# Kernel optimization log

Hardware: AMD Instinct MI355X
Metric: run time of the kernel (lower is better)

## Reference

```python
import jax, jax.numpy as jnp
import numpy as np

B, D, L, K = 8, 256, 2048, 24
R = L // 2 + 1  # rfft bins
H = 2 * D      # mlp hidden
EPS = 1e-5


def setup_inputs() -> dict:
    key = jax.random.key(0)
    ks = jax.random.split(key, 10)
    s_theta = 1.0 / np.sqrt(D)   # ~kaiming_uniform scale
    s_w1 = 1.0 / np.sqrt(D)
    s_w2 = 1.0 / np.sqrt(H)
    return {
        "x": jax.random.normal(ks[0], (B, D, L), dtype=jnp.float32),
        "Phi_f_re": jax.random.normal(ks[1], (K, R), dtype=jnp.float32),
        "Phi_f_im": jax.random.normal(ks[2], (K, R), dtype=jnp.float32),
        "Theta": jax.random.uniform(ks[3], (K, D, D), jnp.float32, -s_theta, s_theta),
        "gamma": jnp.ones((D,), jnp.float32),
        "beta": jnp.zeros((D,), jnp.float32),
        "W1": jax.random.uniform(ks[4], (H, D), jnp.float32, -s_w1, s_w1),
        "b1": jax.random.uniform(ks[5], (H,), jnp.float32, -s_w1, s_w1),
        "W2": jax.random.uniform(ks[6], (D, H), jnp.float32, -s_w2, s_w2),
        "b2": jax.random.uniform(ks[7], (D,), jnp.float32, -s_w2, s_w2),
    }


def reference(x, Phi_f_re, Phi_f_im, Theta, gamma, beta, W1, b1, W2, b2):
    # x: [B, D, L]. LayerNorm over channel dim D (torch norms last dim of x.transpose(1,2)).
    mu = jnp.mean(x, axis=1, keepdims=True)
    var = jnp.var(x, axis=1, keepdims=True)
    z = (x - mu) * jax.lax.rsqrt(var + EPS) * gamma[None, :, None] + beta[None, :, None]

    Xf = jnp.fft.rfft(z, axis=-1)                       # [B, D, R] complex
    Phi_c = Phi_f_re - 1j * Phi_f_im                    # conj(Phi_f), [K, R]
    # Sf[b,h,r] = sum_{d,k} Xf[b,d,r] * conj(Phi)[k,r] * Theta[k,h,d]
    # (identical to the torch real/imag split since Theta is real)
    Sf = jnp.einsum('bdr,kr,khd->bhr', Xf, Phi_c, Theta)
    S = jnp.fft.irfft(Sf, n=L, axis=-1)                 # [B, D, L]

    # 1x1 Conv1d MLP with exact GELU
    h = jax.nn.gelu(jnp.einsum('hd,bdl->bhl', W1, S) + b1[None, :, None], approximate=False)
    out = jnp.einsum('dh,bhl->bdl', W2, h) + b2[None, :, None]
    return x + out
```

## Files before the change

### kernel.cpp

```cpp
#include <hip/hip_runtime.h>
#include <hip/hip_bf16.h>
#include <hip/hip_fp16.h>
#include <math.h>

#define BB 8
#define DD 256
#define LL 2048
#define KK 24
#define RR 1025
#define HH 512

typedef __attribute__((ext_vector_type(8))) _Float16 f16x8;
typedef __attribute__((ext_vector_type(4))) float f32x4;

__device__ __forceinline__ unsigned short f2h(float f) {
  return __builtin_bit_cast(unsigned short, __float2half_rn(f));
}

__global__ void ln_kernel(const float* __restrict__ x, const float* __restrict__ gamma,
                          const float* __restrict__ beta, float* __restrict__ z) {
  __shared__ float red[2][4][64];
  __shared__ float mu_s[64], rs_s[64];
  int blk = blockIdx.x;
  int b = blk >> 5;
  int l0 = (blk & 31) << 6;
  int t = threadIdx.x;
  int ll = t & 63;
  int part = t >> 6;
  int l = l0 + ll;
  const float* xb = x + ((size_t)b * DD) * LL + l;
  float xv[64];
  float s = 0.f, ss = 0.f;
  #pragma unroll
  for (int i = 0; i < 64; ++i) {
    float v = xb[(size_t)(part * 64 + i) * LL];
    xv[i] = v; s += v; ss += v * v;
  }
  red[0][part][ll] = s; red[1][part][ll] = ss;
  __syncthreads();
  if (part == 0) {
    float S = red[0][0][ll] + red[0][1][ll] + red[0][2][ll] + red[0][3][ll];
    float Q = red[1][0][ll] + red[1][1][ll] + red[1][2][ll] + red[1][3][ll];
    float mu = S * (1.f / 256.f);
    float var = Q * (1.f / 256.f) - mu * mu;
    mu_s[ll] = mu; rs_s[ll] = rsqrtf(var + 1e-5f);
  }
  __syncthreads();
  float mu = mu_s[ll], rs = rs_s[ll];
  float* zb = z + ((size_t)b * DD) * LL + l;
  #pragma unroll
  for (int i = 0; i < 64; ++i) {
    int d = part * 64 + i;
    zb[(size_t)d * LL] = (xv[i] - mu) * rs * gamma[d] + beta[d];
  }
}

__global__ void theta_prep(const float* __restrict__ Theta, unsigned* __restrict__ A2u) {
  int bi = blockIdx.x;
  int k = bi >> 8, h = bi & 255;
  int t = threadIdx.x;
  float2 v = *reinterpret_cast<const float2*>(Theta + (size_t)k * 65536 + h * 256 + 2 * t);
  A2u[(size_t)h * 3072 + k * 128 + t] =
      __builtin_bit_cast(unsigned, __floats2half2_rn(v.x, v.y));
}

__global__ void w_prep(const float* __restrict__ W1, const float* __restrict__ W2,
                       unsigned* __restrict__ W1h, unsigned* __restrict__ W2h) {
  int i = blockIdx.x * 256 + threadIdx.x;
  float2 a = reinterpret_cast<const float2*>(W1)[i];
  W1h[i] = __builtin_bit_cast(unsigned, __floats2half2_rn(a.x, a.y));
  float2 b = reinterpret_cast<const float2*>(W2)[i];
  W2h[i] = __builtin_bit_cast(unsigned, __floats2half2_rn(b.x, b.y));
}

__device__ __forceinline__ float2* fft2048(float2* bufA, float2* bufB,
                                           const float2* __restrict__ tw, int t) {
  float2* src = bufA; float2* dst = bufB;
  for (int stage = 0; stage < 11; ++stage) {
    int s = 1 << stage;
    #pragma unroll
    for (int j = 0; j < 4; ++j) {
      int idx = t + 256 * j;
      int q = idx & (s - 1);
      int p = idx >> stage;
      float2 a = src[idx];
      float2 b = src[idx + 1024];
      float sr = a.x + b.x, si = a.y + b.y;
      float dr = a.x - b.x, di = a.y - b.y;
      float2 w = tw[p << stage];
      dst[q + 2 * s * p] = make_float2(sr, si);
      dst[q + 2 * s * p + s] = make_float2(dr * w.x - di * w.y, dr * w.y + di * w.x);
    }
    __syncthreads();
    float2* tmp = src; src = dst; dst = tmp;
  }
  return src;
}

__device__ __forceinline__ void build_tw(float2* tw, int t) {
  #pragma unroll
  for (int j = 0; j < 4; ++j) {
    int i = t + 256 * j;
    float xfrac = (float)i * (1.f / 1024.f);
    tw[i] = make_float2(cospif(xfrac), -sinpif(xfrac));
  }
}

__global__ void rfft_kernel(const float* __restrict__ z, unsigned* __restrict__ Xf2) {
  __shared__ float2 bufA[2048];
  __shared__ float2 bufB[2048];
  __shared__ float2 tw[1024];
  int row = blockIdx.x;
  int t = threadIdx.x;
  build_tw(tw, t);
  const float* zr = z + (size_t)row * LL;
  #pragma unroll
  for (int j = 0; j < 8; ++j) {
    int i = t + 256 * j;
    bufA[i] = make_float2(zr[i], 0.f);
  }
  __syncthreads();
  float2* res = fft2048(bufA, bufB, tw, t);
  #pragma unroll
  for (int j = 0; j < 5; ++j) {
    int r = t + 256 * j;
    if (r <= 1024) {
      float2 v = res[r];
      Xf2[(size_t)row * RR + r] = __builtin_bit_cast(unsigned, __floats2half2_rn(v.x, v.y));
    }
  }
}

__global__ void irfft_kernel(const float2* __restrict__ Sf, float* __restrict__ S) {
  __shared__ float2 bufA[2048];
  __shared__ float2 bufB[2048];
  __shared__ float2 tw[1024];
  int row = blockIdx.x;
  int t = threadIdx.x;
  build_tw(tw, t);
  const float2* fr = Sf + (size_t)row * RR;
  #pragma unroll
  for (int j = 0; j < 8; ++j) {
    int i = t + 256 * j;
    float2 v;
    if (i <= 1024) { v = fr[i]; v.y = -v.y; }
    else           { v = fr[2048 - i]; }
    bufA[i] = v;
  }
  __syncthreads();
  float2* res = fft2048(bufA, bufB, tw, t);
  const float scale = 1.f / 2048.f;
  float* sr = S + (size_t)row * LL;
  #pragma unroll
  for (int j = 0; j < 8; ++j) {
    int i = t + 256 * j;
    sr[i] = res[i].x * scale;
  }
}

#define SPEC_BUILD(kk, dss, bbuf)                                              \
  {                                                                            \
    int d2l_ = t & 15;                                                         \
    int pp_ = t >> 4;                                                          \
    _Pragma("unroll")                                                          \
    for (int j_ = 0; j_ < 2; ++j_) {                                           \
      int p_ = pp_ + 16 * j_;                                                  \
      int rl_ = p_ >> 3, bb_ = p_ & 7;                                         \
      unsigned xr_ = xs_r[(dss) * 16 + d2l_][rl_ * 8 + bb_];                   \
      unsigned xi_ = xs_i[(dss) * 16 + d2l_][rl_ * 8 + bb_];                   \
      __half2 pr_ = __builtin_bit_cast(__half2, phi_pr[kk][rl_]);              \
      __half2 pi_ = __builtin_bit_cast(__half2, phi_pi[kk][rl_]);              \
      __half2 xrh_ = __builtin_bit_cast(__half2, xr_);                         \
      __half2 xih_ = __builtin_bit_cast(__half2, xi_);                         \
      __half2 re_ = __hfma2(xrh_, pr_, __hmul2(xih_, pi_));                    \
      __half2 im_ = __hfma2(xih_, pr_, __hneg2(__hmul2(xrh_, pi_)));           \
      Bl[bbuf][2 * p_][d2l_] = __builtin_bit_cast(unsigned, re_);              \
      Bl[bbuf][2 * p_ + 1][d2l_] = __builtin_bit_cast(unsigned, im_);          \
    }                                                                          \
  }

__global__ void __launch_bounds__(256)
spectral_mfma(const unsigned* __restrict__ Xf2,
              const unsigned short* __restrict__ A2,
              const float* __restrict__ Phi_re,
              const float* __restrict__ Phi_im,
              float2* __restrict__ Sf) {
  __shared__ unsigned xs_r[32][34];
  __shared__ unsigned xs_i[32][34];
  __shared__ alignas(16) unsigned Bl[2][64][20];
  __shared__ unsigned phi_pr[KK][4], phi_pi[KK][4];

  int t = threadIdx.x;
  int lane = t & 63;
  int w = t >> 6;
  int l15 = lane & 15;
  int l4 = lane >> 4;
  int rt = blockIdx.x;
  int r0 = rt << 2;
  int h0 = blockIdx.y << 7;
  int hrow = h0 + w * 32 + l15;

  if (t < 96) {
    int k = t >> 2, rl = t & 3;
    int rc = min(r0 + rl, RR - 1);
    float pr = Phi_re[k * RR + rc], pi = Phi_im[k * RR + rc];
    phi_pr[k][rl] = __builtin_bit_cast(unsigned, __floats2half2_rn(pr, pr));
    phi_pi[k][rl] = __builtin_bit_cast(unsigned, __floats2half2_rn(pi, pi));
  }

  f32x4 acc[2][4];
  #pragma unroll
  for (int fm = 0; fm < 2; ++fm)
    #pragma unroll
    for (int fn = 0; fn < 4; ++fn) acc[fm][fn] = (f32x4){0.f, 0.f, 0.f, 0.f};

  for (int win = 0; win < 4; ++win) {
    __syncthreads();
    #pragma unroll
    for (int e = 0; e < 4; ++e) {
      int idx = t + 256 * e;
      int d2 = idx >> 5, rl = (idx >> 3) & 3, b = idx & 7;
      int d = win * 64 + 2 * d2;
      int rc = min(r0 + rl, RR - 1);
      unsigned u0 = Xf2[(size_t)(b * DD + d) * RR + rc];
      unsigned u1 = Xf2[(size_t)(b * DD + d + 1) * RR + rc];
      xs_r[d2][rl * 8 + b] = (u0 & 0xffffu) | (u1 << 16);
      xs_i[d2][rl * 8 + b] = (u0 >> 16) | (u1 & 0xffff0000u);
    }
    __syncthreads();
    SPEC_BUILD(0, 0, 0);
    __syncthreads();
    for (int cc = 0; cc < 48; ++cc) {
      int k = cc >> 1, ds = cc & 1;
      int kdbase = k * 256 + win * 64 + ds * 32;
      f16x8 af0 = *reinterpret_cast<const f16x8*>(
          A2 + (size_t)hrow * 6144 + kdbase + l4 * 8);
      f16x8 af1 = *reinterpret_cast<const f16x8*>(
          A2 + (size_t)(hrow + 16) * 6144 + kdbase + l4 * 8);
      if (cc < 47) {
        int k2 = (cc + 1) >> 1, ds2 = (cc + 1) & 1, bf2 = (cc + 1) & 1;
        SPEC_BUILD(k2, ds2, bf2);
      }
      int buf = cc & 1;
      #pragma unroll
      for (int fn = 0; fn < 4; ++fn) {
        f16x8 bf = *reinterpret_cast<const f16x8*>(&Bl[buf][fn * 16 + l15][l4 * 4]);
        acc[0][fn] = __builtin_amdgcn_mfma_f32_16x16x32_f16(af0, bf, acc[0][fn], 0, 0, 0);
        acc[1][fn] = __builtin_amdgcn_mfma_f32_16x16x32_f16(af1, bf, acc[1][fn], 0, 0, 0);
      }
      __syncthreads();
    }
  }

  float* Sff = reinterpret_cast<float*>(Sf);
  int b = l15 >> 1, ri = l15 & 1;
  #pragma unroll
  for (int fm = 0; fm < 2; ++fm)
    #pragma unroll
    for (int fn = 0; fn < 4; ++fn) {
      int r = min(r0 + fn, RR - 1);
      #pragma unroll
      for (int i = 0; i < 4; ++i) {
        int h = h0 + w * 32 + fm * 16 + l4 * 4 + i;
        Sff[((((size_t)(b * DD + h)) * RR + r) << 1) + ri] = acc[fm][fn][i];
      }
    }
}

__global__ void __launch_bounds__(256)
mlp_mfma(const float* __restrict__ S, const float* __restrict__ x,
         const unsigned short* __restrict__ W1h,
         const float* __restrict__ b1,
         const unsigned short* __restrict__ W2h,
         const float* __restrict__ b2,
         float* __restrict__ out) {
  __shared__ unsigned short S_lds[64 * 256];
  __shared__ unsigned short H_lds[64 * 128];
  char* Sb = reinterpret_cast<char*>(S_lds);
  char* Hb = reinterpret_cast<char*>(H_lds);

  int t = threadIdx.x;
  int lane = t & 63, w = t >> 6;
  int l15 = lane & 15, l4 = lane >> 4;
  int bb = blockIdx.x >> 5;
  int l0 = (blockIdx.x & 31) << 6;

  {
    int n = t & 63;
    int dbase = t >> 6;
    int n7s = (n & 7) << 4;
    const float* Sp = S + ((size_t)(bb * DD)) * LL + l0 + n;
    #pragma unroll 8
    for (int p = 0; p < 64; ++p) {
      int d = p * 4 + dbase;
      float v = Sp[(size_t)d * LL];
      *reinterpret_cast<unsigned short*>(Sb + n * 512 + ((2 * d) ^ n7s)) = f2h(v);
    }
  }

  f32x4 acc2[4][4];
  #pragma unroll
  for (int fm = 0; fm < 4; ++fm)
    #pragma unroll
    for (int fn = 0; fn < 4; ++fn) acc2[fm][fn] = (f32x4){0.f, 0.f, 0.f, 0.f};

  for (int ch = 0; ch < 4; ++ch) {
    __syncthreads();
    f32x4 acc1[2][4];
    #pragma unroll
    for (int fm = 0; fm < 2; ++fm) {
      float4 b1v = *reinterpret_cast<const float4*>(
          b1 + ch * 128 + w * 32 + fm * 16 + l4 * 4);
      #pragma unroll
      for (int fn = 0; fn < 4; ++fn)
        acc1[fm][fn] = (f32x4){b1v.x, b1v.y, b1v.z, b1v.w};
    }
    #pragma unroll
    for (int ks = 0; ks < 8; ++ks) {
      f16x8 af0 = *reinterpret_cast<const f16x8*>(
          W1h + (size_t)(ch * 128 + w * 32 + l15) * 256 + ks * 32 + l4 * 8);
      f16x8 af1 = *reinterpret_cast<const f16x8*>(
          W1h + (size_t)(ch * 128 + w * 32 + 16 + l15) * 256 + ks * 32 + l4 * 8);
      #pragma unroll
      for (int fn = 0; fn < 4; ++fn) {
        int n = fn * 16 + l15;
        f16x8 bf = *reinterpret_cast<const f16x8*>(
            Sb + n * 512 + ((64 * ks + 16 * l4) ^ ((n & 7) << 4)));
        acc1[0][fn] = __builtin_amdgcn_mfma_f32_16x16x32_f16(af0, bf, acc1[0][fn], 0, 0, 0);
        acc1[1][fn] = __builtin_amdgcn_mfma_f32_16x16x32_f16(af1, bf, acc1[1][fn], 0, 0, 0);
      }
    }
    #pragma unroll
    for (int fm = 0; fm < 2; ++fm)
      #pragma unroll
      for (int fn = 0; fn < 4; ++fn) {
        unsigned short hv[4];
        #pragma unroll
        for (int i = 0; i < 4; ++i) {
          float v = acc1[fm][fn][i];
          hv[i] = f2h(0.5f * v * (1.f + erff(v * 0.70710678118654752f)));
        }
        int n = fn * 16 + l15;
        int hl2 = 2 * (w * 32 + fm * 16 + l4 * 4);
        *reinterpret_cast<uint2*>(Hb + n * 256 + (hl2 ^ ((n & 7) << 4))) =
            *reinterpret_cast<uint2*>(hv);
      }
    __syncthreads();
    #pragma unroll
    for (int ks = 0; ks < 4; ++ks) {
      f16x8 bfv[4];
      #pragma unroll
      for (int fn = 0; fn < 4; ++fn) {
        int n = fn * 16 + l15;
        bfv[fn] = *reinterpret_cast<const f16x8*>(
            Hb + n * 256 + ((64 * ks + 16 * l4) ^ ((n & 7) << 4)));
      }
      #pragma unroll
      for (int fm = 0; fm < 4; ++fm) {
        f16x8 af = *reinterpret_cast<const f16x8*>(
            W2h + (size_t)(w * 64 + fm * 16 + l15) * 512 + ch * 128 + ks * 32 + l4 * 8);
        #pragma unroll
        for (int fn = 0; fn < 4; ++fn)
          acc2[fm][fn] = __builtin_amdgcn_mfma_f32_16x16x32_f16(af, bfv[fn], acc2[fm][fn], 0, 0, 0);
      }
    }
  }

  #pragma unroll
  for (int fm = 0; fm < 4; ++fm) {
    float4 b2v = *reinterpret_cast<const float4*>(b2 + w * 64 + fm * 16 + l4 * 4);
    #pragma unroll
    for (int i = 0; i < 4; ++i) {
      int d = w * 64 + fm * 16 + l4 * 4 + i;
      const float* xr = x + ((size_t)(bb * DD + d)) * LL + l0;
      float* orow = out + ((size_t)(bb * DD + d)) * LL + l0;
      float bias = (i == 0) ? b2v.x : (i == 1) ? b2v.y : (i == 2) ? b2v.z : b2v.w;
      #pragma unroll
      for (int fn = 0; fn < 4; ++fn) {
        int n = fn * 16 + l15;
        orow[n] = xr[n] + bias + acc2[fm][fn][i];
      }
    }
  }
}

extern "C" void kernel_launch(void* const* d_in, const int* in_sizes, int n_in,
                              void* d_out, int out_size, void* d_ws, size_t ws_size,
                              hipStream_t stream) {
  const float* x      = (const float*)d_in[0];
  const float* Phi_re = (const float*)d_in[1];
  const float* Phi_im = (const float*)d_in[2];
  const float* Theta  = (const float*)d_in[3];
  const float* gamma  = (const float*)d_in[4];
  const float* beta   = (const float*)d_in[5];
  const float* W1     = (const float*)d_in[6];
  const float* b1     = (const float*)d_in[7];
  const float* W2     = (const float*)d_in[8];
  const float* b2     = (const float*)d_in[9];

  float* ws = (float*)d_ws;
  float*    z   = ws;
  unsigned* Xf2 = (unsigned*)(ws + 4194304);
  float2*   Sf  = (float2*)(ws + 8392704);
  unsigned* A2u = (unsigned*)(ws + 12591104);
  unsigned* W1h = (unsigned*)(ws + 14163968);
  unsigned* W2h = (unsigned*)(ws + 14295040);

  ln_kernel<<<dim3(BB * (LL / 64)), 256, 0, stream>>>(x, gamma, beta, z);
  theta_prep<<<dim3(KK * 256), 128, 0, stream>>>(Theta, A2u);
  w_prep<<<dim3(256), 256, 0, stream>>>(W1, W2, W1h, W2h);
  rfft_kernel<<<dim3(BB * DD), 256, 0, stream>>>(z, Xf2);
  spectral_mfma<<<dim3(257, 2), 256, 0, stream>>>(
      Xf2, (const unsigned short*)A2u, Phi_re, Phi_im, Sf);
  irfft_kernel<<<dim3(BB * DD), 256, 0, stream>>>(Sf, z);
  mlp_mfma<<<dim3(256), 256, 0, stream>>>(
      z, x, (const unsigned short*)W1h, b1, (const unsigned short*)W2h, b2,
      (float*)d_out);
}
```

Measured before the change: 265.0 us.

## Merge spectral GEMM H-split into 512-thread blocks with 64-wide K steps

The spectral MFMA kernel now runs one 512-thread block (8 waves) per 4-bin frequency tile covering all 256 output channels, where before it used two 256-thread blocks split over H. Each step builds a 64-wide d-slice of the Phi-modulated spectrum in LDS, so there are 24 barrier-separated steps per window instead of 48. This is meant to halve redundant Xf loads and spectrum construction and to cut synchronisation. The cost is fewer blocks (257) on a large GPU, which may leave compute units idle, and more register pressure from the extra A fragments.

```diff
diff --git a/kernel.cpp b/kernel.cpp
--- a/kernel.cpp
+++ b/kernel.cpp
@@ -158,28 +158,7 @@
   }
 }
 
-#define SPEC_BUILD(kk, dss, bbuf)                                              \
-  {                                                                            \
-    int d2l_ = t & 15;                                                         \
-    int pp_ = t >> 4;                                                          \
-    _Pragma("unroll")                                                          \
-    for (int j_ = 0; j_ < 2; ++j_) {                                           \
-      int p_ = pp_ + 16 * j_;                                                  \
-      int rl_ = p_ >> 3, bb_ = p_ & 7;                                         \
-      unsigned xr_ = xs_r[(dss) * 16 + d2l_][rl_ * 8 + bb_];                   \
-      unsigned xi_ = xs_i[(dss) * 16 + d2l_][rl_ * 8 + bb_];                   \
-      __half2 pr_ = __builtin_bit_cast(__half2, phi_pr[kk][rl_]);              \
-      __half2 pi_ = __builtin_bit_cast(__half2, phi_pi[kk][rl_]);              \
-      __half2 xrh_ = __builtin_bit_cast(__half2, xr_);                         \
-      __half2 xih_ = __builtin_bit_cast(__half2, xi_);                         \
-      __half2 re_ = __hfma2(xrh_, pr_, __hmul2(xih_, pi_));                    \
-      __half2 im_ = __hfma2(xih_, pr_, __hneg2(__hmul2(xrh_, pi_)));           \
-      Bl[bbuf][2 * p_][d2l_] = __builtin_bit_cast(unsigned, re_);              \
-      Bl[bbuf][2 * p_ + 1][d2l_] = __builtin_bit_cast(unsigned, im_);          \
-    }                                                                          \
-  }
-
-__global__ void __launch_bounds__(256)
+__global__ void __launch_bounds__(512)
 spectral_mfma(const unsigned* __restrict__ Xf2,
               const unsigned short* __restrict__ A2,
               const float* __restrict__ Phi_re,
@@ -187,7 +166,7 @@
               float2* __restrict__ Sf) {
   __shared__ unsigned xs_r[32][34];
   __shared__ unsigned xs_i[32][34];
-  __shared__ alignas(16) unsigned Bl[2][64][20];
+  __shared__ alignas(16) unsigned Bl[2][64][40];
   __shared__ unsigned phi_pr[KK][4], phi_pi[KK][4];
 
   int t = threadIdx.x;
@@ -195,10 +174,12 @@
   int w = t >> 6;
   int l15 = lane & 15;
   int l4 = lane >> 4;
-  int rt = blockIdx.x;
-  int r0 = rt << 2;
-  int h0 = blockIdx.y << 7;
-  int hrow = h0 + w * 32 + l15;
+  int r0 = blockIdx.x << 2;
+
+  int bc = t & 31;
+  int r16 = t >> 5;
+  int bbq = r16 >> 1;
+  int bri = r16 & 1;
 
   if (t < 96) {
     int k = t >> 2, rl = t & 3;
@@ -214,11 +195,30 @@
     #pragma unroll
     for (int fn = 0; fn < 4; ++fn) acc[fm][fn] = (f32x4){0.f, 0.f, 0.f, 0.f};
 
+  const unsigned short* Arow0 = A2 + (size_t)(w * 32 + l15) * 6144 + l4 * 8;
+  const unsigned short* Arow1 = Arow0 + (size_t)16 * 6144;
+
+  #define SPEC_BUILD64(kk, bbuf)                                               \
+    {                                                                          \
+      _Pragma("unroll")                                                        \
+      for (int j_ = 0; j_ < 4; ++j_) {                                         \
+        unsigned xr_ = xs_r[bc][j_ * 8 + bbq];                                 \
+        unsigned xi_ = xs_i[bc][j_ * 8 + bbq];                                 \
+        __half2 pr_ = __builtin_bit_cast(__half2, phi_pr[kk][j_]);             \
+        __half2 pi_ = __builtin_bit_cast(__half2, phi_pi[kk][j_]);             \
+        __half2 xrh_ = __builtin_bit_cast(__half2, xr_);                       \
+        __half2 xih_ = __builtin_bit_cast(__half2, xi_);                       \
+        __half2 re_ = __hfma2(xrh_, pr_, __hmul2(xih_, pi_));                  \
+        __half2 im_ = __hfma2(xih_, pr_, __hneg2(__hmul2(xrh_, pi_)));         \
+        Bl[bbuf][r16 + 16 * j_][bc] = __builtin_bit_cast(unsigned, bri ? im_ : re_); \
+      }                                                                        \
+    }
+
   for (int win = 0; win < 4; ++win) {
     __syncthreads();
     #pragma unroll
-    for (int e = 0; e < 4; ++e) {
-      int idx = t + 256 * e;
+    for (int e = 0; e < 2; ++e) {
+      int idx = t + 512 * e;
       int d2 = idx >> 5, rl = (idx >> 3) & 3, b = idx & 7;
       int d = win * 64 + 2 * d2;
       int rc = min(r0 + rl, RR - 1);
@@ -228,25 +228,28 @@
       xs_i[d2][rl * 8 + b] = (u0 >> 16) | (u1 & 0xffff0000u);
     }
     __syncthreads();
-    SPEC_BUILD(0, 0, 0);
-    __syncthreads();
-    for (int cc = 0; cc < 48; ++cc) {
-      int k = cc >> 1, ds = cc & 1;
-      int kdbase = k * 256 + win * 64 + ds * 32;
-      f16x8 af0 = *reinterpret_cast<const f16x8*>(
-          A2 + (size_t)hrow * 6144 + kdbase + l4 * 8);
-      f16x8 af1 = *reinterpret_cast<const f16x8*>(
-          A2 + (size_t)(hrow + 16) * 6144 + kdbase + l4 * 8);
-      if (cc < 47) {
-        int k2 = (cc + 1) >> 1, ds2 = (cc + 1) & 1, bf2 = (cc + 1) & 1;
-        SPEC_BUILD(k2, ds2, bf2);
-      }
-      int buf = cc & 1;
+    SPEC_BUILD64(0, 0);
+    __syncthreads();
+    #pragma unroll
+    for (int k = 0; k < 24; ++k) {
+      const int buf = k & 1;
+      const size_t kcol = (size_t)k * 256 + win * 64;
+      f16x8 a00 = *reinterpret_cast<const f16x8*>(Arow0 + kcol);
+      f16x8 a10 = *reinterpret_cast<const f16x8*>(Arow1 + kcol);
+      f16x8 a01 = *reinterpret_cast<const f16x8*>(Arow0 + kcol + 32);
+      f16x8 a11 = *reinterpret_cast<const f16x8*>(Arow1 + kcol + 32);
+      if (k < 23) SPEC_BUILD64(k + 1, (k + 1) & 1);
       #pragma unroll
       for (int fn = 0; fn < 4; ++fn) {
         f16x8 bf = *reinterpret_cast<const f16x8*>(&Bl[buf][fn * 16 + l15][l4 * 4]);
-        acc[0][fn] = __builtin_amdgcn_mfma_f32_16x16x32_f16(af0, bf, acc[0][fn], 0, 0, 0);
-        acc[1][fn] = __builtin_amdgcn_mfma_f32_16x16x32_f16(af1, bf, acc[1][fn], 0, 0, 0);
+        acc[0][fn] = __builtin_amdgcn_mfma_f32_16x16x32_f16(a00, bf, acc[0][fn], 0, 0, 0);
+        acc[1][fn] = __builtin_amdgcn_mfma_f32_16x16x32_f16(a10, bf, acc[1][fn], 0, 0, 0);
+      }
+      #pragma unroll
+      for (int fn = 0; fn < 4; ++fn) {
+        f16x8 bf = *reinterpret_cast<const f16x8*>(&Bl[buf][fn * 16 + l15][16 + l4 * 4]);
+        acc[0][fn] = __builtin_amdgcn_mfma_f32_16x16x32_f16(a01, bf, acc[0][fn], 0, 0, 0);
+        acc[1][fn] = __builtin_amdgcn_mfma_f32_16x16x32_f16(a11, bf, acc[1][fn], 0, 0, 0);
       }
       __syncthreads();
     }
@@ -261,10 +264,11 @@
       int r = min(r0 + fn, RR - 1);
       #pragma unroll
       for (int i = 0; i < 4; ++i) {
-        int h = h0 + w * 32 + fm * 16 + l4 * 4 + i;
+        int h = w * 32 + fm * 16 + l4 * 4 + i;
         Sff[((((size_t)(b * DD + h)) * RR + r) << 1) + ri] = acc[fm][fn][i];
       }
     }
+  #undef SPEC_BUILD64
 }
 
 __global__ void __launch_bounds__(256)
@@ -410,7 +414,7 @@
   theta_prep<<<dim3(KK * 256), 128, 0, stream>>>(Theta, A2u);
   w_prep<<<dim3(256), 256, 0, stream>>>(W1, W2, W1h, W2h);
   rfft_kernel<<<dim3(BB * DD), 256, 0, stream>>>(z, Xf2);
-  spectral_mfma<<<dim3(257, 2), 256, 0, stream>>>(
+  spectral_mfma<<<dim3(257), 512, 0, stream>>>(
       Xf2, (const unsigned short*)A2u, Phi_re, Phi_im, Sf);
   irfft_kernel<<<dim3(BB * DD), 256, 0, stream>>>(Sf, z);
   mlp_mfma<<<dim3(256), 256, 0, stream>>>(
```

Result: slower. 306.7 us (+15.7%).

## Split spectral reduction over channel windows and sum partials in irfft

Applied to the files above, without the earlier changes.

The spectral MFMA kernel gains a grid z dimension of 2, and each slice reduces half of the d-windows into its own partial spectrum buffer. The irfft kernel sums the two partials while loading, which folds the split-K reduction into an existing pass. The aim is to double the number of blocks in the spectral GEMM for better CU occupancy. In exchange it writes and reads an extra full complex spectrum buffer. The workspace is repacked so one partial aliases the LayerNorm buffer, and irfft writes its output in place with a 2050-float row stride that matches the partial-spectrum row size.

```diff
diff --git a/kernel.cpp b/kernel.cpp
--- a/kernel.cpp
+++ b/kernel.cpp
@@ -9,6 +9,7 @@
 #define KK 24
 #define RR 1025
 #define HH 512
+#define SSTR 2050
 
 typedef __attribute__((ext_vector_type(8))) _Float16 f16x8;
 typedef __attribute__((ext_vector_type(4))) float f32x4;
@@ -131,26 +132,34 @@
   }
 }
 
-__global__ void irfft_kernel(const float2* __restrict__ Sf, float* __restrict__ S) {
+__global__ void irfft_kernel(const float2* __restrict__ Sf0,
+                             const float2* __restrict__ Sf1,
+                             float* __restrict__ S) {
   __shared__ float2 bufA[2048];
   __shared__ float2 bufB[2048];
   __shared__ float2 tw[1024];
   int row = blockIdx.x;
   int t = threadIdx.x;
   build_tw(tw, t);
-  const float2* fr = Sf + (size_t)row * RR;
+  const float2* fr0 = Sf0 + (size_t)row * RR;
+  const float2* fr1 = Sf1 + (size_t)row * RR;
   #pragma unroll
   for (int j = 0; j < 8; ++j) {
     int i = t + 256 * j;
     float2 v;
-    if (i <= 1024) { v = fr[i]; v.y = -v.y; }
-    else           { v = fr[2048 - i]; }
+    if (i <= 1024) {
+      float2 a = fr0[i], b = fr1[i];
+      v = make_float2(a.x + b.x, -(a.y + b.y));
+    } else {
+      float2 a = fr0[2048 - i], b = fr1[2048 - i];
+      v = make_float2(a.x + b.x, a.y + b.y);
+    }
     bufA[i] = v;
   }
   __syncthreads();
   float2* res = fft2048(bufA, bufB, tw, t);
   const float scale = 1.f / 2048.f;
-  float* sr = S + (size_t)row * LL;
+  float* sr = S + (size_t)row * SSTR;
   #pragma unroll
   for (int j = 0; j < 8; ++j) {
     int i = t + 256 * j;
@@ -184,7 +193,8 @@
               const unsigned short* __restrict__ A2,
               const float* __restrict__ Phi_re,
               const float* __restrict__ Phi_im,
-              float2* __restrict__ Sf) {
+              float2* __restrict__ Sf0,
+              float2* __restrict__ Sf1) {
   __shared__ unsigned xs_r[32][34];
   __shared__ unsigned xs_i[32][34];
   __shared__ alignas(16) unsigned Bl[2][64][20];
@@ -198,6 +208,7 @@
   int rt = blockIdx.x;
   int r0 = rt << 2;
   int h0 = blockIdx.y << 7;
+  int wz = blockIdx.z;
   int hrow = h0 + w * 32 + l15;
 
   if (t < 96) {
@@ -214,7 +225,7 @@
     #pragma unroll
     for (int fn = 0; fn < 4; ++fn) acc[fm][fn] = (f32x4){0.f, 0.f, 0.f, 0.f};
 
-  for (int win = 0; win < 4; ++win) {
+  for (int win = wz * 2; win < wz * 2 + 2; ++win) {
     __syncthreads();
     #pragma unroll
     for (int e = 0; e < 4; ++e) {
@@ -252,7 +263,7 @@
     }
   }
 
-  float* Sff = reinterpret_cast<float*>(Sf);
+  float* Sff = reinterpret_cast<float*>(wz ? Sf1 : Sf0);
   int b = l15 >> 1, ri = l15 & 1;
   #pragma unroll
   for (int fm = 0; fm < 2; ++fm)
@@ -289,11 +300,11 @@
     int n = t & 63;
     int dbase = t >> 6;
     int n7s = (n & 7) << 4;
-    const float* Sp = S + ((size_t)(bb * DD)) * LL + l0 + n;
+    const float* Sp = S + ((size_t)(bb * DD)) * SSTR + l0 + n;
     #pragma unroll 8
     for (int p = 0; p < 64; ++p) {
       int d = p * 4 + dbase;
-      float v = Sp[(size_t)d * LL];
+      float v = Sp[(size_t)d * SSTR];
       *reinterpret_cast<unsigned short*>(Sb + n * 512 + ((2 * d) ^ n7s)) = f2h(v);
     }
   }
@@ -399,21 +410,22 @@
   const float* b2     = (const float*)d_in[9];
 
   float* ws = (float*)d_ws;
-  float*    z   = ws;
-  unsigned* Xf2 = (unsigned*)(ws + 4194304);
-  float2*   Sf  = (float2*)(ws + 8392704);
-  unsigned* A2u = (unsigned*)(ws + 12591104);
-  unsigned* W1h = (unsigned*)(ws + 14163968);
-  unsigned* W2h = (unsigned*)(ws + 14295040);
+  float*    z    = ws;
+  float2*   Sf1  = (float2*)ws;
+  unsigned* Xf2  = (unsigned*)(ws + 4198400);
+  float2*   Sf0  = (float2*)(ws + 6297600);
+  unsigned* A2u  = (unsigned*)(ws + 10496000);
+  unsigned* W1h  = (unsigned*)(ws + 11282432);
+  unsigned* W2h  = (unsigned*)(ws + 11347968);
 
   ln_kernel<<<dim3(BB * (LL / 64)), 256, 0, stream>>>(x, gamma, beta, z);
   theta_prep<<<dim3(KK * 256), 128, 0, stream>>>(Theta, A2u);
   w_prep<<<dim3(256), 256, 0, stream>>>(W1, W2, W1h, W2h);
   rfft_kernel<<<dim3(BB * DD), 256, 0, stream>>>(z, Xf2);
-  spectral_mfma<<<dim3(257, 2), 256, 0, stream>>>(
-      Xf2, (const unsigned short*)A2u, Phi_re, Phi_im, Sf);
-  irfft_kernel<<<dim3(BB * DD), 256, 0, stream>>>(Sf, z);
+  spectral_mfma<<<dim3(257, 2, 2), 256, 0, stream>>>(
+      Xf2, (const unsigned short*)A2u, Phi_re, Phi_im, Sf0, Sf1);
+  irfft_kernel<<<dim3(BB * DD), 256, 0, stream>>>(Sf0, Sf1, ws);
   mlp_mfma<<<dim3(256), 256, 0, stream>>>(
-      z, x, (const unsigned short*)W1h, b1, (const unsigned short*)W2h, b2,
+      ws, x, (const unsigned short*)W1h, b1, (const unsigned short*)W2h, b2,
       (float*)d_out);
 }
```

New measurement: 280.0 us. +5.7%, slower.

## Retile spectral MFMA kernel to cover all H rows with two frequency bins per block

Applied to the files above, without the earlier changes.

The spectral GEMM block tile changes from 128 h-rows by 4 frequency bins to all 256 h-rows by 2 frequency bins. Each wave now holds 4x2 accumulator fragments instead of 2x4, and the grid goes from 257x2 to 513 blocks. The spectral B tile is built with one element per thread, and the Xf staging in LDS is halved. This removes the redundant Xf load and spectral-build work across the two h-halves, but every block still streams the full Theta A matrix for fewer bins, so A-operand traffic per unit of output grows.

```diff
diff --git a/kernel.cpp b/kernel.cpp
--- a/kernel.cpp
+++ b/kernel.cpp
@@ -160,23 +160,18 @@
 
 #define SPEC_BUILD(kk, dss, bbuf)                                              \
   {                                                                            \
-    int d2l_ = t & 15;                                                         \
-    int pp_ = t >> 4;                                                          \
-    _Pragma("unroll")                                                          \
-    for (int j_ = 0; j_ < 2; ++j_) {                                           \
-      int p_ = pp_ + 16 * j_;                                                  \
-      int rl_ = p_ >> 3, bb_ = p_ & 7;                                         \
-      unsigned xr_ = xs_r[(dss) * 16 + d2l_][rl_ * 8 + bb_];                   \
-      unsigned xi_ = xs_i[(dss) * 16 + d2l_][rl_ * 8 + bb_];                   \
-      __half2 pr_ = __builtin_bit_cast(__half2, phi_pr[kk][rl_]);              \
-      __half2 pi_ = __builtin_bit_cast(__half2, phi_pi[kk][rl_]);              \
-      __half2 xrh_ = __builtin_bit_cast(__half2, xr_);                         \
-      __half2 xih_ = __builtin_bit_cast(__half2, xi_);                         \
-      __half2 re_ = __hfma2(xrh_, pr_, __hmul2(xih_, pi_));                    \
-      __half2 im_ = __hfma2(xih_, pr_, __hneg2(__hmul2(xrh_, pi_)));           \
-      Bl[bbuf][2 * p_][d2l_] = __builtin_bit_cast(unsigned, re_);              \
-      Bl[bbuf][2 * p_ + 1][d2l_] = __builtin_bit_cast(unsigned, im_);          \
-    }                                                                          \
+    int rl_ = p_ >> 3, bb_ = p_ & 7;                                           \
+    unsigned xr_ = xs_r[(dss) * 16 + bc][p_];                                  \
+    unsigned xi_ = xs_i[(dss) * 16 + bc][p_];                                  \
+    __half2 pr_ = __builtin_bit_cast(__half2, phi_pr[kk][rl_]);                \
+    __half2 pi_ = __builtin_bit_cast(__half2, phi_pi[kk][rl_]);                \
+    __half2 xrh_ = __builtin_bit_cast(__half2, xr_);                           \
+    __half2 xih_ = __builtin_bit_cast(__half2, xi_);                           \
+    __half2 re_ = __hfma2(xrh_, pr_, __hmul2(xih_, pi_));                      \
+    __half2 im_ = __hfma2(xih_, pr_, __hneg2(__hmul2(xrh_, pi_)));             \
+    Bl[bbuf][2 * p_][bc] = __builtin_bit_cast(unsigned, re_);                  \
+    Bl[bbuf][2 * p_ + 1][bc] = __builtin_bit_cast(unsigned, im_);              \
+    (void)bb_;                                                                 \
   }
 
 __global__ void __launch_bounds__(256)
@@ -185,10 +180,10 @@
               const float* __restrict__ Phi_re,
               const float* __restrict__ Phi_im,
               float2* __restrict__ Sf) {
-  __shared__ unsigned xs_r[32][34];
-  __shared__ unsigned xs_i[32][34];
-  __shared__ alignas(16) unsigned Bl[2][64][20];
-  __shared__ unsigned phi_pr[KK][4], phi_pi[KK][4];
+  __shared__ unsigned xs_r[32][18];
+  __shared__ unsigned xs_i[32][18];
+  __shared__ alignas(16) unsigned Bl[2][32][20];
+  __shared__ unsigned phi_pr[KK][2], phi_pi[KK][2];
 
   int t = threadIdx.x;
   int lane = t & 63;
@@ -196,36 +191,42 @@
   int l15 = lane & 15;
   int l4 = lane >> 4;
   int rt = blockIdx.x;
-  int r0 = rt << 2;
-  int h0 = blockIdx.y << 7;
-  int hrow = h0 + w * 32 + l15;
-
-  if (t < 96) {
-    int k = t >> 2, rl = t & 3;
+  int r0 = rt << 1;
+  int hrow = w * 64 + l15;
+
+  int bc = t & 15;
+  int p_ = t >> 4;
+
+  if (t < 48) {
+    int k = t >> 1, rl = t & 1;
     int rc = min(r0 + rl, RR - 1);
     float pr = Phi_re[k * RR + rc], pi = Phi_im[k * RR + rc];
     phi_pr[k][rl] = __builtin_bit_cast(unsigned, __floats2half2_rn(pr, pr));
     phi_pi[k][rl] = __builtin_bit_cast(unsigned, __floats2half2_rn(pi, pi));
   }
 
-  f32x4 acc[2][4];
-  #pragma unroll
-  for (int fm = 0; fm < 2; ++fm)
-    #pragma unroll
-    for (int fn = 0; fn < 4; ++fn) acc[fm][fn] = (f32x4){0.f, 0.f, 0.f, 0.f};
+  f32x4 acc[4][2];
+  #pragma unroll
+  for (int fm = 0; fm < 4; ++fm)
+    #pragma unroll
+    for (int fn = 0; fn < 2; ++fn) acc[fm][fn] = (f32x4){0.f, 0.f, 0.f, 0.f};
+
+  const unsigned short* Arow = A2 + (size_t)hrow * 6144 + l4 * 8;
 
   for (int win = 0; win < 4; ++win) {
     __syncthreads();
     #pragma unroll
-    for (int e = 0; e < 4; ++e) {
+    for (int e = 0; e < 2; ++e) {
       int idx = t + 256 * e;
-      int d2 = idx >> 5, rl = (idx >> 3) & 3, b = idx & 7;
+      int d2 = idx >> 4;
+      int r8b = idx & 15;
+      int rl = r8b >> 3, b = r8b & 7;
       int d = win * 64 + 2 * d2;
       int rc = min(r0 + rl, RR - 1);
       unsigned u0 = Xf2[(size_t)(b * DD + d) * RR + rc];
       unsigned u1 = Xf2[(size_t)(b * DD + d + 1) * RR + rc];
-      xs_r[d2][rl * 8 + b] = (u0 & 0xffffu) | (u1 << 16);
-      xs_i[d2][rl * 8 + b] = (u0 >> 16) | (u1 & 0xffff0000u);
+      xs_r[d2][r8b] = (u0 & 0xffffu) | (u1 << 16);
+      xs_i[d2][r8b] = (u0 >> 16) | (u1 & 0xffff0000u);
     }
     __syncthreads();
     SPEC_BUILD(0, 0, 0);
@@ -233,20 +234,22 @@
     for (int cc = 0; cc < 48; ++cc) {
       int k = cc >> 1, ds = cc & 1;
       int kdbase = k * 256 + win * 64 + ds * 32;
-      f16x8 af0 = *reinterpret_cast<const f16x8*>(
-          A2 + (size_t)hrow * 6144 + kdbase + l4 * 8);
-      f16x8 af1 = *reinterpret_cast<const f16x8*>(
-          A2 + (size_t)(hrow + 16) * 6144 + kdbase + l4 * 8);
+      f16x8 af0 = *reinterpret_cast<const f16x8*>(Arow + kdbase);
+      f16x8 af1 = *reinterpret_cast<const f16x8*>(Arow + (size_t)16 * 6144 + kdbase);
+      f16x8 af2 = *reinterpret_cast<const f16x8*>(Arow + (size_t)32 * 6144 + kdbase);
+      f16x8 af3 = *reinterpret_cast<const f16x8*>(Arow + (size_t)48 * 6144 + kdbase);
       if (cc < 47) {
         int k2 = (cc + 1) >> 1, ds2 = (cc + 1) & 1, bf2 = (cc + 1) & 1;
         SPEC_BUILD(k2, ds2, bf2);
       }
       int buf = cc & 1;
       #pragma unroll
-      for (int fn = 0; fn < 4; ++fn) {
+      for (int fn = 0; fn < 2; ++fn) {
         f16x8 bf = *reinterpret_cast<const f16x8*>(&Bl[buf][fn * 16 + l15][l4 * 4]);
         acc[0][fn] = __builtin_amdgcn_mfma_f32_16x16x32_f16(af0, bf, acc[0][fn], 0, 0, 0);
         acc[1][fn] = __builtin_amdgcn_mfma_f32_16x16x32_f16(af1, bf, acc[1][fn], 0, 0, 0);
+        acc[2][fn] = __builtin_amdgcn_mfma_f32_16x16x32_f16(af2, bf, acc[2][fn], 0, 0, 0);
+        acc[3][fn] = __builtin_amdgcn_mfma_f32_16x16x32_f16(af3, bf, acc[3][fn], 0, 0, 0);
       }
       __syncthreads();
     }
@@ -255,13 +258,13 @@
   float* Sff = reinterpret_cast<float*>(Sf);
   int b = l15 >> 1, ri = l15 & 1;
   #pragma unroll
-  for (int fm = 0; fm < 2; ++fm)
-    #pragma unroll
-    for (int fn = 0; fn < 4; ++fn) {
+  for (int fm = 0; fm < 4; ++fm)
+    #pragma unroll
+    for (int fn = 0; fn < 2; ++fn) {
       int r = min(r0 + fn, RR - 1);
       #pragma unroll
       for (int i = 0; i < 4; ++i) {
-        int h = h0 + w * 32 + fm * 16 + l4 * 4 + i;
+        int h = w * 64 + fm * 16 + l4 * 4 + i;
         Sff[((((size_t)(b * DD + h)) * RR + r) << 1) + ri] = acc[fm][fn][i];
       }
     }
@@ -410,7 +413,7 @@
   theta_prep<<<dim3(KK * 256), 128, 0, stream>>>(Theta, A2u);
   w_prep<<<dim3(256), 256, 0, stream>>>(W1, W2, W1h, W2h);
   rfft_kernel<<<dim3(BB * DD), 256, 0, stream>>>(z, Xf2);
-  spectral_mfma<<<dim3(257, 2), 256, 0, stream>>>(
+  spectral_mfma<<<dim3(513), 256, 0, stream>>>(
       Xf2, (const unsigned short*)A2u, Phi_re, Phi_im, Sf);
   irfft_kernel<<<dim3(BB * DD), 256, 0, stream>>>(Sf, z);
   mlp_mfma<<<dim3(256), 256, 0, stream>>>(
```

Result: slower. 377.9 us (+42.6%).
